# Optimization experiments

Measured on AMD Instinct MI355X. Metric: run time of the kernel, lower is better.

## Reference

```python
import jax, jax.numpy as jnp
import numpy as np

D = 1024
N_HEADS = 16
D_HEAD = D // N_HEADS


def setup_inputs() -> dict:
    key = jax.random.key(0)
    ks = jax.random.split(key, 7)
    B, S = 4, 1024
    x = jax.random.normal(ks[0], (B, S, D), dtype=jnp.float32)
    # per-head linear params, stacked over heads: W[h] is [d_head, d_head] (torch Linear weight),
    # y = s @ W[h].T + b[h]
    scale = 1.0 / np.sqrt(D_HEAD)
    Wq = jax.random.uniform(ks[1], (N_HEADS, D_HEAD, D_HEAD), jnp.float32, -scale, scale)
    Wk = jax.random.uniform(ks[2], (N_HEADS, D_HEAD, D_HEAD), jnp.float32, -scale, scale)
    Wv = jax.random.uniform(ks[3], (N_HEADS, D_HEAD, D_HEAD), jnp.float32, -scale, scale)
    bq = jax.random.uniform(ks[4], (N_HEADS, D_HEAD), jnp.float32, -scale, scale)
    bk = jax.random.uniform(ks[5], (N_HEADS, D_HEAD), jnp.float32, -scale, scale)
    bv = jax.random.uniform(ks[6], (N_HEADS, D_HEAD), jnp.float32, -scale, scale)
    return {"pix_sequences": x, "Wq": Wq, "Wk": Wk, "Wv": Wv,
            "bq": bq, "bk": bk, "bv": bv}


def reference(pix_sequences, Wq, Wk, Wv, bq, bk, bv):
    B, S, d = pix_sequences.shape
    # split feature dim into heads: [B, S, H, dh]
    xh = pix_sequences.reshape(B, S, N_HEADS, D_HEAD)
    # per-head linear: y = s @ W.T + b
    q = jnp.einsum('bshd,hed->bshe', xh, Wq) + bq  # [B,S,H,dh]
    k = jnp.einsum('bshd,hed->bshe', xh, Wk) + bk
    v = jnp.einsum('bshd,hed->bshe', xh, Wv) + bv
    scores = jnp.einsum('bqhd,bkhd->bhqk', q, k) / jnp.sqrt(jnp.float32(D_HEAD))
    attn = jax.nn.softmax(scores, axis=-1)  # [B,H,S,S]
    out = jnp.einsum('bhqk,bkhd->bqhd', attn, v)  # [B,S,H,dh]
    return out.reshape(B, S, d)
```

## Files before the change

### kernel.cpp

```cpp
#include <hip/hip_runtime.h>
#include <hip/hip_bf16.h>

constexpr int BB = 4;
constexpr int SS = 1024;
constexpr int HH = 16;
constexpr int DH = 64;
constexpr int DM = 1024;

using f32x16 = __attribute__((ext_vector_type(16))) float;
using s16x8  = __attribute__((ext_vector_type(8))) short;

__device__ __forceinline__ f32x16 mfma32(s16x8 a, s16x8 b, f32x16 c) {
    return __builtin_amdgcn_mfma_f32_32x32x16_bf16(a, b, c, 0, 0, 0);
}

__device__ __forceinline__ unsigned short bf16bits(float x) {
    union { __hip_bfloat16 h; unsigned short s; } cv;
    cv.h = __float2bfloat16(x);
    return cv.s;
}
__device__ __forceinline__ unsigned pk_bf16(float lo, float hi) {
    return (unsigned)bf16bits(lo) | ((unsigned)bf16bits(hi) << 16);
}

__device__ __forceinline__ float fast_exp2(float x) {
#if __has_builtin(__builtin_amdgcn_exp2f)
    return __builtin_amdgcn_exp2f(x);
#else
    return __expf(x * 0.6931471805599453f);
#endif
}

__device__ __forceinline__ int kperm(int g) {
    const int m = g & 12;
    return (m == 4 || m == 8) ? (g ^ 12) : g;
}

__global__ __launch_bounds__(256) void w_pack_kernel(
    const float* __restrict__ Wq, const float* __restrict__ Wk, const float* __restrict__ Wv,
    __hip_bfloat16* __restrict__ wfrag)
{
    const int gid = blockIdx.x * 256 + threadIdx.x;
    const int e = gid & 63;
    const int m = (gid >> 6) % 3;
    const int h = gid / 192;
    const float* Wm = (m == 0) ? Wq : (m == 1) ? Wk : Wv;
    const float* src = Wm + (size_t)(h * DH + e) * DH;
    s16x8* dst = reinterpret_cast<s16x8*>(wfrag);
    #pragma unroll
    for (int s = 0; s < 4; ++s) {
        #pragma unroll
        for (int hi = 0; hi < 2; ++hi) {
            const float* p = src + s * 16 + hi * 8;
            float4 a  = reinterpret_cast<const float4*>(p)[0];
            float4 b4 = reinterpret_cast<const float4*>(p)[1];
            union { unsigned u[4]; s16x8 v; } f;
            f.u[0] = pk_bf16(a.x, a.y);   f.u[1] = pk_bf16(a.z, a.w);
            f.u[2] = pk_bf16(b4.x, b4.y); f.u[3] = pk_bf16(b4.z, b4.w);
            dst[(((h * 3 + m) * 4 + s) * 2 + hi) * 64 + e] = f.v;
        }
    }
}

__global__ __launch_bounds__(256) void qkv_proj_kernel(
    const float* __restrict__ x,
    const __hip_bfloat16* __restrict__ wfrag,
    const float* __restrict__ bq, const float* __restrict__ bk, const float* __restrict__ bv,
    __hip_bfloat16* __restrict__ q_ws, __hip_bfloat16* __restrict__ k_ws,
    __hip_bfloat16* __restrict__ v_ws)
{
    const int bid  = blockIdx.x;
    const int tile = bid & 7;
    const int pair = bid >> 3;
    const int b = pair >> 4, h = pair & 15;
    const int t = threadIdx.x;
    const int w = t >> 6, l = t & 63;
    const int lq = l & 31, hi = l >> 5;
    const int s0 = tile * 128;

    __shared__ __align__(16) char Xs[16384];
    __shared__ __align__(16) char Kt[16384];
    __shared__ __align__(16) char Vt[16384];

    {
        const float* xb = x + (size_t)(b * SS + s0) * DM + h * DH;
        #pragma unroll
        for (int i = 0; i < 8; ++i) {
            const int c  = t + 256 * i;
            const int r  = c >> 4, cw = c & 15;
            float4 v4 = *reinterpret_cast<const float4*>(xb + (size_t)r * DM + cw * 4);
            uint2 p;
            p.x = pk_bf16(v4.x, v4.y);
            p.y = pk_bf16(v4.z, v4.w);
            *reinterpret_cast<uint2*>(Xs + r * 128 + ((cw * 8) ^ ((r & 7) << 4))) = p;
        }
    }
    __syncthreads();

    const int arow = w * 32 + lq;
    const int asw  = (arow & 7) << 4;
    s16x8 af[4];
    #pragma unroll
    for (int s = 0; s < 4; ++s)
        af[s] = *reinterpret_cast<const s16x8*>(Xs + arow * 128 + ((s * 32 + hi * 16) ^ asw));
    __syncthreads();

    const s16x8* wfp = reinterpret_cast<const s16x8*>(wfrag);

    #pragma unroll
    for (int m = 0; m < 3; ++m) {
        const float* bm = (m == 0) ? bq : (m == 1) ? bk : bv;

        f32x16 a0, a1;
        #pragma unroll
        for (int r = 0; r < 16; ++r) { a0[r] = 0.0f; a1[r] = 0.0f; }

        #pragma unroll
        for (int s = 0; s < 4; ++s) {
            const int wb = (((h * 3 + m) * 4 + s) * 2 + hi) * 64;
            s16x8 bf0 = wfp[wb + lq];
            s16x8 bf1 = wfp[wb + 32 + lq];
            a0 = mfma32(af[s], bf0, a0);
            a1 = mfma32(af[s], bf1, a1);
        }

        const float bias0 = bm[h * DH + lq];
        const float bias1 = bm[h * DH + 32 + lq];

        if (m < 2) {
            char* T = (m == 0) ? Xs : Kt;
            #pragma unroll
            for (int r = 0; r < 16; ++r) {
                const int row = w * 32 + (r & 3) + 8 * (r >> 2) + 4 * hi;
                const int sw  = (row & 7) << 4;
                *reinterpret_cast<unsigned short*>(T + row * 128 + ((lq * 2) ^ sw)) =
                    bf16bits(a0[r] + bias0);
                *reinterpret_cast<unsigned short*>(T + row * 128 + (((32 + lq) * 2) ^ sw)) =
                    bf16bits(a1[r] + bias1);
            }
        } else {
            #pragma unroll
            for (int g = 0; g < 4; ++g) {
                const int off = w * 64 + g * 16 + hi * 8;
                uint2 p0, p1;
                p0.x = pk_bf16(a0[4*g+0] + bias0, a0[4*g+1] + bias0);
                p0.y = pk_bf16(a0[4*g+2] + bias0, a0[4*g+3] + bias0);
                p1.x = pk_bf16(a1[4*g+0] + bias1, a1[4*g+1] + bias1);
                p1.y = pk_bf16(a1[4*g+2] + bias1, a1[4*g+3] + bias1);
                *reinterpret_cast<uint2*>(Vt + lq * 256 + (off ^ ((lq & 7) << 4))) = p0;
                *reinterpret_cast<uint2*>(Vt + (32 + lq) * 256 + (off ^ (((32 + lq) & 7) << 4))) = p1;
            }
        }
    }
    __syncthreads();

    #pragma unroll
    for (int i = 0; i < 4; ++i) {
        const int c   = t + 256 * i;
        const int row = c >> 3, cc = c & 7;
        const int off = row * 128 + ((cc * 16) ^ ((row & 7) << 4));
        s16x8 qv = *reinterpret_cast<const s16x8*>(Xs + off);
        *reinterpret_cast<s16x8*>(q_ws + ((size_t)pair * SS + s0 + row) * DH + cc * 8) = qv;
        s16x8 kv = *reinterpret_cast<const s16x8*>(Kt + off);
        *reinterpret_cast<s16x8*>(k_ws + ((size_t)pair * SS + s0 + row) * DH + cc * 8) = kv;
    }
    #pragma unroll
    for (int i = 0; i < 4; ++i) {
        const int c   = t + 256 * i;
        const int row = c >> 4, cc = c & 15;
        s16x8 vv = *reinterpret_cast<const s16x8*>(
            Vt + row * 256 + ((cc * 16) ^ ((row & 7) << 4)));
        *reinterpret_cast<s16x8*>(v_ws + ((size_t)pair * DH + row) * SS + s0 + cc * 8) = vv;
    }
}

__global__ __launch_bounds__(512, 4) void attn_kernel(
    const __hip_bfloat16* __restrict__ q_ws,
    const __hip_bfloat16* __restrict__ k_ws,
    const __hip_bfloat16* __restrict__ v_ws,
    float* __restrict__ out)
{
    const int bid  = blockIdx.x;
    const int lbid = (bid & 7) * 64 + (bid >> 3);
    const int qt   = lbid & 7;
    const int pair = lbid >> 3;
    const int b = pair >> 4, h = pair & 15;
    const int t = threadIdx.x;
    const int w = t >> 6, l = t & 63;
    const int lq = l & 31, hi = l >> 5;
    const int qg = w & 3, p = w >> 2;

    __shared__ __align__(16) char smem[33792];

    const __hip_bfloat16* qp =
        q_ws + ((size_t)pair * SS + qt * 128 + qg * 32 + lq) * DH + hi * 8;
    s16x8 qf[4];
    #pragma unroll
    for (int s5 = 0; s5 < 4; ++s5)
        qf[s5] = *reinterpret_cast<const s16x8*>(qp + s5 * 16);

    const int u0 = t, u1 = t + 512;
    const __hip_bfloat16* kb = k_ws + (size_t)pair * SS * DH;
    const __hip_bfloat16* vb = v_ws + (size_t)pair * DH * SS;

    const int r0g = (u0 >> 3) & 31, r0m = r0g & 12;
    const int pr0 = (u0 >> 3 & ~31) | ((r0m == 4 || r0m == 8) ? (r0g ^ 12) : r0g);
    const int kOff0 = pr0 * 128 + (((u0 & 7) ^ (pr0 & 7)) << 4);
    const int r1g = (u1 >> 3) & 31, r1m = r1g & 12;
    const int pr1 = (u1 >> 3 & ~31) | ((r1m == 4 || r1m == 8) ? (r1g ^ 12) : r1g);
    const int kOff1 = pr1 * 128 + (((u1 & 7) ^ (pr1 & 7)) << 4);

    const int vOff0 = (u0 >> 4) * 256 + (((u0 & 15) ^ ((u0 >> 4) & 15)) << 4);
    const int vOff1 = (u1 >> 4) * 256 + (((u1 & 15) ^ ((u1 >> 4) & 15)) << 4);
    const size_t vs0 = (size_t)(u0 >> 4) * SS + (u0 & 15) * 8;
    const size_t vs1 = (size_t)(u1 >> 4) * SS + (u1 & 15) * 8;

    {
        s16x8 k0 = *reinterpret_cast<const s16x8*>(kb + u0 * 8);
        s16x8 k1 = *reinterpret_cast<const s16x8*>(kb + u1 * 8);
        s16x8 v0 = *reinterpret_cast<const s16x8*>(vb + vs0);
        s16x8 v1 = *reinterpret_cast<const s16x8*>(vb + vs1);
        *reinterpret_cast<s16x8*>(smem + kOff0) = k0;
        *reinterpret_cast<s16x8*>(smem + kOff1) = k1;
        *reinterpret_cast<s16x8*>(smem + 16384 + vOff0) = v0;
        *reinterpret_cast<s16x8*>(smem + 16384 + vOff1) = v1;
    }
    __syncthreads();

    f32x16 o0, o1, lacc;
    #pragma unroll
    for (int r = 0; r < 16; ++r) { o0[r] = 0.0f; o1[r] = 0.0f; lacc[r] = 0.0f; }
    const float cml = 0.18033688011112042f;

    const int kbase0 = (p * 64 + lq) * 128;
    const int kbase1 = kbase0 + 32 * 128;
    const int swzK = (lq & 7) << 4;
    const int swzV = (lq & 15) << 4;
    const int vrow0 = lq * 256, vrow1 = (32 + lq) * 256;

    s16x8 kr0, kr1, vr0, vr1;
    for (int st = 0; st < 8; ++st) {
        if (st < 7) {
            kr0 = *reinterpret_cast<const s16x8*>(kb + (st + 1) * 8192 + u0 * 8);
            kr1 = *reinterpret_cast<const s16x8*>(kb + (st + 1) * 8192 + u1 * 8);
            vr0 = *reinterpret_cast<const s16x8*>(vb + vs0 + (st + 1) * 128);
            vr1 = *reinterpret_cast<const s16x8*>(vb + vs1 + (st + 1) * 128);
        }
        const char* Kp = smem;
        const char* Vp = smem + 16384;

        f32x16 sc0, sc1;
        #pragma unroll
        for (int r = 0; r < 16; ++r) { sc0[r] = 0.0f; sc1[r] = 0.0f; }
        #pragma unroll
        for (int s5 = 0; s5 < 4; ++s5) {
            const int co = (2 * s5 + hi) << 4;
            s16x8 ka = *reinterpret_cast<const s16x8*>(Kp + kbase0 + (co ^ swzK));
            sc0 = mfma32(ka, qf[s5], sc0);
        }
        #pragma unroll
        for (int s5 = 0; s5 < 4; ++s5) {
            const int co = (2 * s5 + hi) << 4;
            s16x8 ka = *reinterpret_cast<const s16x8*>(Kp + kbase1 + (co ^ swzK));
            sc1 = mfma32(ka, qf[s5], sc1);
        }

        #pragma unroll
        for (int r = 0; r < 16; ++r) {
            sc0[r] = fast_exp2(sc0[r] * cml);
            sc1[r] = fast_exp2(sc1[r] * cml);
            lacc[r] += sc0[r] + sc1[r];
        }

        #pragma unroll
        for (int s5 = 0; s5 < 4; ++s5) {
            const int base = (s5 & 1) * 8;
            union { unsigned u[4]; s16x8 v; } afr;
            if (s5 < 2) {
                afr.u[0] = pk_bf16(sc0[base + 0], sc0[base + 1]);
                afr.u[1] = pk_bf16(sc0[base + 2], sc0[base + 3]);
                afr.u[2] = pk_bf16(sc0[base + 4], sc0[base + 5]);
                afr.u[3] = pk_bf16(sc0[base + 6], sc0[base + 7]);
            } else {
                afr.u[0] = pk_bf16(sc1[base + 0], sc1[base + 1]);
                afr.u[1] = pk_bf16(sc1[base + 2], sc1[base + 3]);
                afr.u[2] = pk_bf16(sc1[base + 4], sc1[base + 5]);
                afr.u[3] = pk_bf16(sc1[base + 6], sc1[base + 7]);
            }
            const int co = (2 * s5 + hi) << 4;
            s16x8 vb0 = *reinterpret_cast<const s16x8*>(Vp + vrow0 + ((p * 128 + co) ^ swzV));
            o0 = mfma32(afr.v, vb0, o0);
            s16x8 vb1 = *reinterpret_cast<const s16x8*>(Vp + vrow1 + ((p * 128 + co) ^ swzV));
            o1 = mfma32(afr.v, vb1, o1);
        }

        __syncthreads();
        if (st < 7) {
            *reinterpret_cast<s16x8*>(smem + kOff0) = kr0;
            *reinterpret_cast<s16x8*>(smem + kOff1) = kr1;
            *reinterpret_cast<s16x8*>(smem + 16384 + vOff0) = vr0;
            *reinterpret_cast<s16x8*>(smem + 16384 + vOff1) = vr1;
            __syncthreads();
        }
    }

    float ts[16];
    #pragma unroll
    for (int r = 0; r < 16; ++r) ts[r] = lacc[r];
    #pragma unroll
    for (int s = 8; s >= 1; s >>= 1)
        #pragma unroll
        for (int r = 0; r < 8; ++r)
            if (r < s) ts[r] += ts[r + s];
    const float lsum = ts[0] + __shfl_xor(ts[0], 32);

    float* Obuf = reinterpret_cast<float*>(smem + qg * 8192);
    float* mlb  = reinterpret_cast<float*>(smem + 32768 + qg * 256);
    if (p == 1) {
        #pragma unroll
        for (int r = 0; r < 16; ++r) {
            const int qr = (r & 3) + 8 * (r >> 2) + 4 * hi;
            Obuf[qr * 64 + lq]      = o0[r];
            Obuf[qr * 64 + 32 + lq] = o1[r];
        }
        mlb[lq] = lsum;
    }
    __syncthreads();
    if (p == 0) {
        const float inv = 1.0f / (lsum + mlb[lq]);
        #pragma unroll
        for (int r = 0; r < 16; ++r) {
            const int qr = (r & 3) + 8 * (r >> 2) + 4 * hi;
            const float invr = __shfl(inv, qr);
            float* op = out + ((size_t)b * SS + qt * 128 + qg * 32 + qr) * DM + h * DH + lq;
            op[0]  = (o0[r] + Obuf[qr * 64 + lq])      * invr;
            op[32] = (o1[r] + Obuf[qr * 64 + 32 + lq]) * invr;
        }
    }
}

extern "C" void kernel_launch(void* const* d_in, const int* in_sizes, int n_in,
                              void* d_out, int out_size, void* d_ws, size_t ws_size,
                              hipStream_t stream) {
    const float* x  = (const float*)d_in[0];
    const float* Wq = (const float*)d_in[1];
    const float* Wk = (const float*)d_in[2];
    const float* Wv = (const float*)d_in[3];
    const float* bq = (const float*)d_in[4];
    const float* bk = (const float*)d_in[5];
    const float* bv = (const float*)d_in[6];
    float* out = (float*)d_out;

    const size_t N = (size_t)BB * HH * SS * DH;
    __hip_bfloat16* q_ws  = (__hip_bfloat16*)d_ws;
    __hip_bfloat16* k_ws  = q_ws + N;
    __hip_bfloat16* v_ws  = k_ws + N;
    __hip_bfloat16* wfrag = v_ws + N;

    w_pack_kernel<<<dim3(12), dim3(256), 0, stream>>>(Wq, Wk, Wv, wfrag);
    qkv_proj_kernel<<<dim3(BB * HH * (SS / 128)), dim3(256), 0, stream>>>(
        x, wfrag, bq, bk, bv, q_ws, k_ws, v_ws);
    attn_kernel<<<dim3(BB * HH * (SS / 64 / 2)), dim3(512), 0, stream>>>(
        q_ws, k_ws, v_ws, out);
}
```

Measured before the change: 48.04 us.

## Store V in MFMA fragment order and load it straight from global memory

The projection kernel now writes V into a pre-swizzled fragment layout that matches the B-operand order of the 32x32x16 MFMA. The attention kernel loads V fragments directly from global memory (L2) into registers instead of staging them through shared memory. This removes the V LDS writes and reads and their share of the shared-memory traffic. In exchange, each wave issues eight global loads per iteration, and these are used in the same iteration without being prefetched, which may expose memory latency.

```diff
diff --git a/kernel.cpp b/kernel.cpp
--- a/kernel.cpp
+++ b/kernel.cpp
@@ -164,20 +164,28 @@
         s16x8 kv = *reinterpret_cast<const s16x8*>(Kt + off);
         *reinterpret_cast<s16x8*>(k_ws + ((size_t)pair * SS + s0 + row) * DH + cc * 8) = kv;
     }
-    #pragma unroll
-    for (int i = 0; i < 4; ++i) {
-        const int c   = t + 256 * i;
-        const int row = c >> 4, cc = c & 15;
-        s16x8 vv = *reinterpret_cast<const s16x8*>(
-            Vt + row * 256 + ((cc * 16) ^ ((row & 7) << 4)));
-        *reinterpret_cast<s16x8*>(v_ws + ((size_t)pair * DH + row) * SS + s0 + cc * 8) = vv;
+    {
+        s16x8* vo = reinterpret_cast<s16x8*>(v_ws);
+        #pragma unroll
+        for (int i = 0; i < 4; ++i) {
+            const int c    = t + 256 * i;
+            const int dl   = c & 31;
+            const int kc   = (c >> 5) & 15;
+            const int half = c >> 9;
+            const int d    = half * 32 + dl;
+            const int off  = d * 256 + ((kc * 16) ^ ((d & 7) << 4));
+            const int gv   = tile * 4 + (kc >> 2);
+            const int fb   = (((pair * 32 + gv) * 2 + half) * 2 + ((kc >> 1) & 1)) * 2 + (kc & 1);
+            s16x8 vv = *reinterpret_cast<const s16x8*>(Vt + off);
+            vo[fb * 32 + dl] = vv;
+        }
     }
 }
 
 __global__ __launch_bounds__(512, 4) void attn_kernel(
     const __hip_bfloat16* __restrict__ q_ws,
     const __hip_bfloat16* __restrict__ k_ws,
-    const __hip_bfloat16* __restrict__ v_ws,
+    const __hip_bfloat16* __restrict__ vfrag,
     float* __restrict__ out)
 {
     const int bid  = blockIdx.x;
@@ -201,7 +209,7 @@
 
     const int u0 = t, u1 = t + 512;
     const __hip_bfloat16* kb = k_ws + (size_t)pair * SS * DH;
-    const __hip_bfloat16* vb = v_ws + (size_t)pair * DH * SS;
+    const s16x8* vfp = reinterpret_cast<const s16x8*>(vfrag);
 
     const int r0g = (u0 >> 3) & 31, r0m = r0g & 12;
     const int pr0 = (u0 >> 3 & ~31) | ((r0m == 4 || r0m == 8) ? (r0g ^ 12) : r0g);
@@ -210,20 +218,11 @@
     const int pr1 = (u1 >> 3 & ~31) | ((r1m == 4 || r1m == 8) ? (r1g ^ 12) : r1g);
     const int kOff1 = pr1 * 128 + (((u1 & 7) ^ (pr1 & 7)) << 4);
 
-    const int vOff0 = (u0 >> 4) * 256 + (((u0 & 15) ^ ((u0 >> 4) & 15)) << 4);
-    const int vOff1 = (u1 >> 4) * 256 + (((u1 & 15) ^ ((u1 >> 4) & 15)) << 4);
-    const size_t vs0 = (size_t)(u0 >> 4) * SS + (u0 & 15) * 8;
-    const size_t vs1 = (size_t)(u1 >> 4) * SS + (u1 & 15) * 8;
-
     {
         s16x8 k0 = *reinterpret_cast<const s16x8*>(kb + u0 * 8);
         s16x8 k1 = *reinterpret_cast<const s16x8*>(kb + u1 * 8);
-        s16x8 v0 = *reinterpret_cast<const s16x8*>(vb + vs0);
-        s16x8 v1 = *reinterpret_cast<const s16x8*>(vb + vs1);
         *reinterpret_cast<s16x8*>(smem + kOff0) = k0;
         *reinterpret_cast<s16x8*>(smem + kOff1) = k1;
-        *reinterpret_cast<s16x8*>(smem + 16384 + vOff0) = v0;
-        *reinterpret_cast<s16x8*>(smem + 16384 + vOff1) = v1;
     }
     __syncthreads();
 
@@ -235,19 +234,25 @@
     const int kbase0 = (p * 64 + lq) * 128;
     const int kbase1 = kbase0 + 32 * 128;
     const int swzK = (lq & 7) << 4;
-    const int swzV = (lq & 15) << 4;
-    const int vrow0 = lq * 256, vrow1 = (32 + lq) * 256;
-
-    s16x8 kr0, kr1, vr0, vr1;
+
     for (int st = 0; st < 8; ++st) {
+        s16x8 kr0, kr1;
         if (st < 7) {
             kr0 = *reinterpret_cast<const s16x8*>(kb + (st + 1) * 8192 + u0 * 8);
             kr1 = *reinterpret_cast<const s16x8*>(kb + (st + 1) * 8192 + u1 * 8);
-            vr0 = *reinterpret_cast<const s16x8*>(vb + vs0 + (st + 1) * 128);
-            vr1 = *reinterpret_cast<const s16x8*>(vb + vs1 + (st + 1) * 128);
-        }
+        }
+
+        const size_t vbase = ((size_t)(pair * 32 + st * 4 + 2 * p) * 8) * 32 + lq;
+        s16x8 va0 = vfp[vbase + (size_t)(0  + hi) * 32];
+        s16x8 va1 = vfp[vbase + (size_t)(2  + hi) * 32];
+        s16x8 va2 = vfp[vbase + (size_t)(4  + hi) * 32];
+        s16x8 va3 = vfp[vbase + (size_t)(6  + hi) * 32];
+        s16x8 vb0 = vfp[vbase + (size_t)(8  + hi) * 32];
+        s16x8 vb1 = vfp[vbase + (size_t)(10 + hi) * 32];
+        s16x8 vb2 = vfp[vbase + (size_t)(12 + hi) * 32];
+        s16x8 vb3 = vfp[vbase + (size_t)(14 + hi) * 32];
+
         const char* Kp = smem;
-        const char* Vp = smem + 16384;
 
         f32x16 sc0, sc1;
         #pragma unroll
@@ -271,35 +276,29 @@
             sc1[r] = fast_exp2(sc1[r] * cml);
             lacc[r] += sc0[r] + sc1[r];
         }
-
-        #pragma unroll
-        for (int s5 = 0; s5 < 4; ++s5) {
-            const int base = (s5 & 1) * 8;
-            union { unsigned u[4]; s16x8 v; } afr;
-            if (s5 < 2) {
-                afr.u[0] = pk_bf16(sc0[base + 0], sc0[base + 1]);
-                afr.u[1] = pk_bf16(sc0[base + 2], sc0[base + 3]);
-                afr.u[2] = pk_bf16(sc0[base + 4], sc0[base + 5]);
-                afr.u[3] = pk_bf16(sc0[base + 6], sc0[base + 7]);
-            } else {
-                afr.u[0] = pk_bf16(sc1[base + 0], sc1[base + 1]);
-                afr.u[1] = pk_bf16(sc1[base + 2], sc1[base + 3]);
-                afr.u[2] = pk_bf16(sc1[base + 4], sc1[base + 5]);
-                afr.u[3] = pk_bf16(sc1[base + 6], sc1[base + 7]);
-            }
-            const int co = (2 * s5 + hi) << 4;
-            s16x8 vb0 = *reinterpret_cast<const s16x8*>(Vp + vrow0 + ((p * 128 + co) ^ swzV));
-            o0 = mfma32(afr.v, vb0, o0);
-            s16x8 vb1 = *reinterpret_cast<const s16x8*>(Vp + vrow1 + ((p * 128 + co) ^ swzV));
-            o1 = mfma32(afr.v, vb1, o1);
-        }
+        union { unsigned u[4]; s16x8 v; } af0, af1, af2, af3;
+        af0.u[0] = pk_bf16(sc0[0],  sc0[1]);  af0.u[1] = pk_bf16(sc0[2],  sc0[3]);
+        af0.u[2] = pk_bf16(sc0[4],  sc0[5]);  af0.u[3] = pk_bf16(sc0[6],  sc0[7]);
+        af1.u[0] = pk_bf16(sc0[8],  sc0[9]);  af1.u[1] = pk_bf16(sc0[10], sc0[11]);
+        af1.u[2] = pk_bf16(sc0[12], sc0[13]); af1.u[3] = pk_bf16(sc0[14], sc0[15]);
+        af2.u[0] = pk_bf16(sc1[0],  sc1[1]);  af2.u[1] = pk_bf16(sc1[2],  sc1[3]);
+        af2.u[2] = pk_bf16(sc1[4],  sc1[5]);  af2.u[3] = pk_bf16(sc1[6],  sc1[7]);
+        af3.u[0] = pk_bf16(sc1[8],  sc1[9]);  af3.u[1] = pk_bf16(sc1[10], sc1[11]);
+        af3.u[2] = pk_bf16(sc1[12], sc1[13]); af3.u[3] = pk_bf16(sc1[14], sc1[15]);
+
+        o0 = mfma32(af0.v, va0, o0);
+        o1 = mfma32(af0.v, va2, o1);
+        o0 = mfma32(af1.v, va1, o0);
+        o1 = mfma32(af1.v, va3, o1);
+        o0 = mfma32(af2.v, vb0, o0);
+        o1 = mfma32(af2.v, vb2, o1);
+        o0 = mfma32(af3.v, vb1, o0);
+        o1 = mfma32(af3.v, vb3, o1);
 
         __syncthreads();
         if (st < 7) {
             *reinterpret_cast<s16x8*>(smem + kOff0) = kr0;
             *reinterpret_cast<s16x8*>(smem + kOff1) = kr1;
-            *reinterpret_cast<s16x8*>(smem + 16384 + vOff0) = vr0;
-            *reinterpret_cast<s16x8*>(smem + 16384 + vOff1) = vr1;
             __syncthreads();
         }
     }
```

After: 52.82 us. +9.9%, slower.
